# Kernel optimization log

Hardware: AMD Instinct MI355X
Metric: run time of the kernel (lower is better)

The kernel has to match this reference:

```python
import jax, jax.numpy as jnp
import numpy as np
from jax import lax


def _rnn_scan(x, Wih, Whh, bih, bhh):
    """Elman RNN: h_t = tanh(x_t @ Wih^T + bih + h_{t-1} @ Whh^T + bhh).
    x: (B, T, I). Returns (last_hidden (B,H), all_hidden (B,T,H))."""
    B = x.shape[0]
    H = Whh.shape[0]
    xs = jnp.swapaxes(x, 0, 1)  # (T, B, I)
    h0 = jnp.zeros((B, H), dtype=x.dtype)

    def step(h, xt):
        h_new = jnp.tanh(xt @ Wih.T + bih + h @ Whh.T + bhh)
        return h_new, h_new

    last, hs = lax.scan(step, h0, xs)
    return last, jnp.swapaxes(hs, 0, 1)  # (B,H), (B,T,H)


def setup_inputs() -> dict:
    key = jax.random.key(0)
    ks = jax.random.split(key, 12)
    B, T = 4096, 256
    I1, H1, H2 = 1, 5, 100
    s1 = 1.0 / np.sqrt(H1)
    s2 = 1.0 / np.sqrt(H2)
    inp = {
        "x": jax.random.normal(ks[0], (B, T, I1), dtype=jnp.float32),
        "Wih1": jax.random.uniform(ks[1], (H1, I1), jnp.float32, -s1, s1),
        "Whh1": jax.random.uniform(ks[2], (H1, H1), jnp.float32, -s1, s1),
        "bih1": jax.random.uniform(ks[3], (H1,), jnp.float32, -s1, s1),
        "bhh1": jax.random.uniform(ks[4], (H1,), jnp.float32, -s1, s1),
        "Wih2": jax.random.uniform(ks[5], (H2, H1), jnp.float32, -s2, s2),
        "Whh2": jax.random.uniform(ks[6], (H2, H2), jnp.float32, -s2, s2),
        "bih2": jax.random.uniform(ks[7], (H2,), jnp.float32, -s2, s2),
        "bhh2": jax.random.uniform(ks[8], (H2,), jnp.float32, -s2, s2),
        "W3": jax.random.uniform(ks[9], (1, H2), jnp.float32, -s2, s2),
        "b3": jax.random.uniform(ks[10], (1,), jnp.float32, -s2, s2),
    }
    return inp


def reference(x, Wih1, Whh1, bih1, bhh1, Wih2, Whh2, bih2, bhh2, W3, b3):
    # layer_1: out = last hidden (B,5), hidden = full sequence (B,T,5)
    _, h1_seq = _rnn_scan(x, Wih1, Whh1, bih1, bhh1)
    # layer_2 consumes the hidden sequence of layer_1
    out2, _ = _rnn_scan(h1_seq, Wih2, Whh2, bih2, bhh2)  # (B,100)
    # final linear + relu
    return jax.nn.relu(out2 @ W3.T + b3)  # (B,1)
```

## Files before the change

kernel.cpp:

```cpp
#include <hip/hip_runtime.h>
#include <stdint.h>

#define T_STEPS 256
#define H1 5
#define H2 100
#define NSTR 16
#define MT 7
#define KT 4
#define ME 112
#define KE 128
#define XPAD 260
#define NW 8
#define NTHR (NW * 64)

typedef _Float16 f16;
typedef _Float16 half8 __attribute__((ext_vector_type(8)));
typedef _Float16 f16x2 __attribute__((ext_vector_type(2)));
typedef float    floatx4 __attribute__((ext_vector_type(4)));

__device__ __forceinline__ int sidx(int k, int n) {
    return ((k >> 5) << 9) + (((k >> 3) & 3) << 7) + (n << 3) + (k & 7);
}

__device__ __forceinline__ float fast_tanh(float v) {
    float e = __expf(2.0f * v);
    return 1.0f - 2.0f * __builtin_amdgcn_rcpf(e + 1.0f);
}

__device__ __forceinline__ uint32_t pkf16(float a, float b) {
    f16x2 v; v.x = (f16)a; v.y = (f16)b;
    return __builtin_bit_cast(uint32_t, v);
}

__global__ __launch_bounds__(NTHR, 1) void rnn_mfma8(
    const float* __restrict__ x,
    const float* __restrict__ Wih1, const float* __restrict__ Whh1,
    const float* __restrict__ bih1, const float* __restrict__ bhh1,
    const float* __restrict__ Wih2, const float* __restrict__ Whh2,
    const float* __restrict__ bih2, const float* __restrict__ bhh2,
    const float* __restrict__ W3,   const float* __restrict__ b3,
    float* __restrict__ out)
{
    const int tid  = threadIdx.x;
    const int lane = tid & 63;
    const int wid  = tid >> 6;
    const int n    = lane & 15;
    const int g    = lane >> 4;
    const int bbase = blockIdx.x * NSTR;

    __shared__ __align__(16) f16   Wlds[ME][KE];
    __shared__ __align__(16) float xs[NSTR][XPAD];
    __shared__ __align__(16) f16   st[2][2048];
    __shared__ float pp[NW][NSTR];

    {
        uint32_t* w32 = (uint32_t*)&Wlds[0][0];
        #pragma unroll
        for (int i = 0; i < 14; ++i) w32[tid + NTHR * i] = 0u;
        const float4* xg = (const float4*)(x + (size_t)bbase * T_STEPS);
        #pragma unroll
        for (int i = 0; i < 2; ++i) {
            const int gi = tid + NTHR * i;
            *(float4*)&xs[gi >> 6][4 * (gi & 63)] = xg[gi];
        }
    }
    __syncthreads();
    for (int i = tid; i < H2 * H2; i += NTHR) Wlds[i / H2][i % H2] = (f16)Whh2[i];
    for (int i = tid; i < H2 * H1; i += NTHR) Wlds[i / H1][H2 + i % H1] = (f16)Wih2[i];
    for (int i = tid; i < H2; i += NTHR)      Wlds[i][105] = (f16)(bih2[i] + bhh2[i]);
    if (tid < H1 * H1) Wlds[H2 + tid / H1][H2 + tid % H1] = (f16)Whh1[tid];
    if (tid < H1) {
        Wlds[H2 + tid][105] = (f16)(bih1[tid] + bhh1[tid]);
        Wlds[H2 + tid][106] = (f16)Wih1[tid];
    }
    {
        uint32_t* s32 = (uint32_t*)&st[0][0];
        #pragma unroll
        for (int i = 0; i < 4; ++i) s32[tid + NTHR * i] = 0u;
    }
    __syncthreads();
    if (tid < NSTR) {
        const float x0 = xs[tid][0];
        #pragma unroll
        for (int c = 0; c < H1; ++c)
            st[0][sidx(H2 + c, tid)] = (f16)fast_tanh(Wih1[c] * x0 + bih1[c] + bhh1[c]);
        st[0][sidx(105, tid)] = (f16)1.0f;
        st[1][sidx(105, tid)] = (f16)1.0f;
        st[0][sidx(106, tid)] = (f16)xs[tid][1];
    }
    half8 Af[KT];
    if (wid < MT) {
        #pragma unroll
        for (int kt = 0; kt < KT; ++kt)
            Af[kt] = *(const half8*)&Wlds[16 * wid + n][32 * kt + 8 * g];
    }
    __syncthreads();

    const int roff = 16 * lane;
    const int woff = ((wid >> 1) << 10) + (((2 * wid + (g >> 1)) & 3) << 8)
                   + (n << 4) + ((g & 1) << 3);
    char* const sp0 = (char*)&st[0][0];
    char* const sp1 = (char*)&st[1][0];
    uint32_t P0 = 0u, P1 = 0u;

    if (wid == 7) {
        f16* const w0 = &st[0][0];
        f16* const w1 = &st[1][0];
        const int si = sidx(106, n);
        #pragma unroll 1
        for (int t2 = 0; t2 < T_STEPS - 2; t2 += 2) {
            if (lane < NSTR) w1[si] = (f16)xs[n][t2 + 2];
            __syncthreads();
            if (lane < NSTR) w0[si] = (f16)xs[n][t2 + 3 < T_STEPS ? t2 + 3 : T_STEPS - 1];
            __syncthreads();
        }
        if (lane < NSTR) w1[si] = (f16)xs[n][T_STEPS - 1];
        __syncthreads();
    } else {
        auto fullstep = [&](const char* rp, char* wp) {
            half8 Bf[KT];
            #pragma unroll
            for (int kt = 0; kt < KT; ++kt)
                Bf[kt] = *(const half8*)(rp + roff + 1024 * kt);

            __builtin_amdgcn_s_setprio(1);
            floatx4 Da = {0.f, 0.f, 0.f, 0.f}, Db = {0.f, 0.f, 0.f, 0.f};
            Da = __builtin_amdgcn_mfma_f32_16x16x32_f16(Af[0], Bf[0], Da, 0, 0, 0);
            Db = __builtin_amdgcn_mfma_f32_16x16x32_f16(Af[2], Bf[2], Db, 0, 0, 0);
            Da = __builtin_amdgcn_mfma_f32_16x16x32_f16(Af[1], Bf[1], Da, 0, 0, 0);
            Db = __builtin_amdgcn_mfma_f32_16x16x32_f16(Af[3], Bf[3], Db, 0, 0, 0);
            const floatx4 D = Da + Db;

            if (wid < 6 || g < 2) {
                const uint32_t q0 = pkf16(fast_tanh(D[0]), fast_tanh(D[1]));
                const uint32_t q1 = pkf16(fast_tanh(D[2]), fast_tanh(D[3]));
                __builtin_amdgcn_s_setprio(0);
                uint2 w; w.x = q0; w.y = q1;
                *(uint2*)(wp + woff) = w;
            } else if (g == 2) {
                const f16 h4 = (f16)fast_tanh(D[0]);
                __builtin_amdgcn_s_setprio(0);
                *(f16*)(wp + 2 * (1664 + 8 * n)) = h4;
            } else {
                __builtin_amdgcn_s_setprio(0);
            }
            __syncthreads();
        };

        #pragma unroll 1
        for (int t2 = 0; t2 < T_STEPS - 2; t2 += 2) {
            fullstep(sp0, sp1);
            fullstep(sp1, sp0);
        }
        fullstep(sp0, sp1);

        half8 Bf[KT];
        #pragma unroll
        for (int kt = 0; kt < KT; ++kt)
            Bf[kt] = *(const half8*)(sp1 + roff + 1024 * kt);
        floatx4 Da = {0.f, 0.f, 0.f, 0.f}, Db = {0.f, 0.f, 0.f, 0.f};
        Da = __builtin_amdgcn_mfma_f32_16x16x32_f16(Af[0], Bf[0], Da, 0, 0, 0);
        Db = __builtin_amdgcn_mfma_f32_16x16x32_f16(Af[2], Bf[2], Db, 0, 0, 0);
        Da = __builtin_amdgcn_mfma_f32_16x16x32_f16(Af[1], Bf[1], Da, 0, 0, 0);
        Db = __builtin_amdgcn_mfma_f32_16x16x32_f16(Af[3], Bf[3], Db, 0, 0, 0);
        const floatx4 D = Da + Db;
        P0 = pkf16(fast_tanh(D[0]), fast_tanh(D[1]));
        P1 = pkf16(fast_tanh(D[2]), fast_tanh(D[3]));
    }

    float p = 0.0f;
    if (wid < MT) {
        const int mbase = 16 * wid + 4 * g;
        if (mbase < H2) {
            const float4 w3v = *(const float4*)(W3 + mbase);
            const f16x2 lo = __builtin_bit_cast(f16x2, P0);
            const f16x2 hi = __builtin_bit_cast(f16x2, P1);
            p += w3v.x * (float)lo.x + w3v.y * (float)lo.y
               + w3v.z * (float)hi.x + w3v.w * (float)hi.y;
        }
    }
    p += __shfl_xor(p, 16);
    p += __shfl_xor(p, 32);
    if (lane < NSTR) pp[wid][n] = p;
    __syncthreads();
    if (tid < NSTR) {
        float s = b3[0];
        #pragma unroll
        for (int w = 0; w < MT; ++w) s += pp[w][tid];
        out[bbase + tid] = fmaxf(s, 0.0f);
    }
}

extern "C" void kernel_launch(void* const* d_in, const int* in_sizes, int n_in,
                              void* d_out, int out_size, void* d_ws, size_t ws_size,
                              hipStream_t stream) {
    const float* x    = (const float*)d_in[0];
    const float* Wih1 = (const float*)d_in[1];
    const float* Whh1 = (const float*)d_in[2];
    const float* bih1 = (const float*)d_in[3];
    const float* bhh1 = (const float*)d_in[4];
    const float* Wih2 = (const float*)d_in[5];
    const float* Whh2 = (const float*)d_in[6];
    const float* bih2 = (const float*)d_in[7];
    const float* bhh2 = (const float*)d_in[8];
    const float* W3   = (const float*)d_in[9];
    const float* b3   = (const float*)d_in[10];
    float* out = (float*)d_out;

    const int B = in_sizes[0] / T_STEPS;
    rnn_mfma8<<<B / NSTR, NTHR, 0, stream>>>(x, Wih1, Whh1, bih1, bhh1,
                                             Wih2, Whh2, bih2, bhh2, W3, b3, out);
}
```

Measured before the change: 83.90 us.

## Halve waves per block, each wave computing two MFMA row tiles per step

Shrinks the block from 8 waves to 4. Three waves each compute two 16-row output tiles per recurrent step, and the fourth wave computes the last tile (the tail of layer 2 plus layer 1) and also writes the next x value, so the dedicated x-feeder wave is gone. The goal is cheaper per-step __syncthreads across fewer waves and more MFMA work per wave between barriers. In exchange, each wave's critical path per step grows (8 MFMAs plus 8 tanh on the busy waves), and the s_setprio hints are dropped.

```diff
diff --git a/kernel.cpp b/kernel.cpp
--- a/kernel.cpp
+++ b/kernel.cpp
@@ -10,7 +10,7 @@
 #define ME 112
 #define KE 128
 #define XPAD 260
-#define NW 8
+#define NW 4
 #define NTHR (NW * 64)
 
 typedef _Float16 f16;
@@ -32,7 +32,9 @@
     return __builtin_bit_cast(uint32_t, v);
 }
 
-__global__ __launch_bounds__(NTHR, 1) void rnn_mfma8(
+#define MFMA(Aa, Bb, Dd) __builtin_amdgcn_mfma_f32_16x16x32_f16((Aa), (Bb), (Dd), 0, 0, 0)
+
+__global__ __launch_bounds__(NTHR, 1) void rnn_mfma4w(
     const float* __restrict__ x,
     const float* __restrict__ Wih1, const float* __restrict__ Whh1,
     const float* __restrict__ bih1, const float* __restrict__ bhh1,
@@ -56,10 +58,10 @@
     {
         uint32_t* w32 = (uint32_t*)&Wlds[0][0];
         #pragma unroll
-        for (int i = 0; i < 14; ++i) w32[tid + NTHR * i] = 0u;
+        for (int i = 0; i < 28; ++i) w32[tid + NTHR * i] = 0u;
         const float4* xg = (const float4*)(x + (size_t)bbase * T_STEPS);
         #pragma unroll
-        for (int i = 0; i < 2; ++i) {
+        for (int i = 0; i < 4; ++i) {
             const int gi = tid + NTHR * i;
             *(float4*)&xs[gi >> 6][4 * (gi & 63)] = xg[gi];
         }
@@ -76,7 +78,7 @@
     {
         uint32_t* s32 = (uint32_t*)&st[0][0];
         #pragma unroll
-        for (int i = 0; i < 4; ++i) s32[tid + NTHR * i] = 0u;
+        for (int i = 0; i < 8; ++i) s32[tid + NTHR * i] = 0u;
     }
     __syncthreads();
     if (tid < NSTR) {
@@ -88,93 +90,133 @@
         st[1][sidx(105, tid)] = (f16)1.0f;
         st[0][sidx(106, tid)] = (f16)xs[tid][1];
     }
-    half8 Af[KT];
-    if (wid < MT) {
+    const int mt0 = 2 * wid;
+    half8 Af0[KT], Af1[KT];
+    #pragma unroll
+    for (int kt = 0; kt < KT; ++kt)
+        Af0[kt] = *(const half8*)&Wlds[16 * mt0 + n][32 * kt + 8 * g];
+    if (wid < 3) {
         #pragma unroll
         for (int kt = 0; kt < KT; ++kt)
-            Af[kt] = *(const half8*)&Wlds[16 * wid + n][32 * kt + 8 * g];
+            Af1[kt] = *(const half8*)&Wlds[16 * (mt0 + 1) + n][32 * kt + 8 * g];
     }
     __syncthreads();
 
     const int roff = 16 * lane;
-    const int woff = ((wid >> 1) << 10) + (((2 * wid + (g >> 1)) & 3) << 8)
-                   + (n << 4) + ((g & 1) << 3);
+    auto woffof = [&](int mt) {
+        return (((4 * mt + g) >> 3) << 10) + (((2 * mt + (g >> 1)) & 3) << 8)
+             + (n << 4) + ((g & 1) << 3);
+    };
+    const int woff0 = woffof(mt0);
+    const int woff1 = woffof(mt0 + 1);
     char* const sp0 = (char*)&st[0][0];
     char* const sp1 = (char*)&st[1][0];
-    uint32_t P0 = 0u, P1 = 0u;
-
-    if (wid == 7) {
-        f16* const w0 = &st[0][0];
-        f16* const w1 = &st[1][0];
-        const int si = sidx(106, n);
-        #pragma unroll 1
-        for (int t2 = 0; t2 < T_STEPS - 2; t2 += 2) {
-            if (lane < NSTR) w1[si] = (f16)xs[n][t2 + 2];
-            __syncthreads();
-            if (lane < NSTR) w0[si] = (f16)xs[n][t2 + 3 < T_STEPS ? t2 + 3 : T_STEPS - 1];
-            __syncthreads();
-        }
-        if (lane < NSTR) w1[si] = (f16)xs[n][T_STEPS - 1];
-        __syncthreads();
-    } else {
-        auto fullstep = [&](const char* rp, char* wp) {
+    uint32_t P0a = 0u, P1a = 0u, P0b = 0u, P1b = 0u;
+
+    if (wid < 3) {
+        auto step2 = [&](const char* rp, char* wp) {
             half8 Bf[KT];
             #pragma unroll
             for (int kt = 0; kt < KT; ++kt)
                 Bf[kt] = *(const half8*)(rp + roff + 1024 * kt);
-
-            __builtin_amdgcn_s_setprio(1);
-            floatx4 Da = {0.f, 0.f, 0.f, 0.f}, Db = {0.f, 0.f, 0.f, 0.f};
-            Da = __builtin_amdgcn_mfma_f32_16x16x32_f16(Af[0], Bf[0], Da, 0, 0, 0);
-            Db = __builtin_amdgcn_mfma_f32_16x16x32_f16(Af[2], Bf[2], Db, 0, 0, 0);
-            Da = __builtin_amdgcn_mfma_f32_16x16x32_f16(Af[1], Bf[1], Da, 0, 0, 0);
-            Db = __builtin_amdgcn_mfma_f32_16x16x32_f16(Af[3], Bf[3], Db, 0, 0, 0);
+            floatx4 Da = {0.f,0.f,0.f,0.f}, Db = {0.f,0.f,0.f,0.f};
+            floatx4 Dc = {0.f,0.f,0.f,0.f}, Dd = {0.f,0.f,0.f,0.f};
+            Da = MFMA(Af0[0], Bf[0], Da);  Dc = MFMA(Af1[0], Bf[0], Dc);
+            Db = MFMA(Af0[2], Bf[2], Db);  Dd = MFMA(Af1[2], Bf[2], Dd);
+            Da = MFMA(Af0[1], Bf[1], Da);  Dc = MFMA(Af1[1], Bf[1], Dc);
+            Db = MFMA(Af0[3], Bf[3], Db);  Dd = MFMA(Af1[3], Bf[3], Dd);
+            const floatx4 D0 = Da + Db, D1 = Dc + Dd;
+            uint2 w0, w1;
+            w0.x = pkf16(fast_tanh(D0[0]), fast_tanh(D0[1]));
+            w0.y = pkf16(fast_tanh(D0[2]), fast_tanh(D0[3]));
+            w1.x = pkf16(fast_tanh(D1[0]), fast_tanh(D1[1]));
+            w1.y = pkf16(fast_tanh(D1[2]), fast_tanh(D1[3]));
+            *(uint2*)(wp + woff0) = w0;
+            *(uint2*)(wp + woff1) = w1;
+            __syncthreads();
+        };
+        #pragma unroll 1
+        for (int t2 = 0; t2 < T_STEPS - 2; t2 += 2) {
+            step2(sp0, sp1);
+            step2(sp1, sp0);
+        }
+        step2(sp0, sp1);
+        half8 Bf[KT];
+        #pragma unroll
+        for (int kt = 0; kt < KT; ++kt)
+            Bf[kt] = *(const half8*)(sp1 + roff + 1024 * kt);
+        floatx4 Da = {0.f,0.f,0.f,0.f}, Db = {0.f,0.f,0.f,0.f};
+        floatx4 Dc = {0.f,0.f,0.f,0.f}, Dd = {0.f,0.f,0.f,0.f};
+        Da = MFMA(Af0[0], Bf[0], Da);  Dc = MFMA(Af1[0], Bf[0], Dc);
+        Db = MFMA(Af0[2], Bf[2], Db);  Dd = MFMA(Af1[2], Bf[2], Dd);
+        Da = MFMA(Af0[1], Bf[1], Da);  Dc = MFMA(Af1[1], Bf[1], Dc);
+        Db = MFMA(Af0[3], Bf[3], Db);  Dd = MFMA(Af1[3], Bf[3], Dd);
+        const floatx4 D0 = Da + Db, D1 = Dc + Dd;
+        P0a = pkf16(fast_tanh(D0[0]), fast_tanh(D0[1]));
+        P1a = pkf16(fast_tanh(D0[2]), fast_tanh(D0[3]));
+        P0b = pkf16(fast_tanh(D1[0]), fast_tanh(D1[1]));
+        P1b = pkf16(fast_tanh(D1[2]), fast_tanh(D1[3]));
+    } else {
+        auto step1 = [&](const char* rp, char* wp, int t) {
+            const int xi = (t + 2 < T_STEPS) ? (t + 2) : (T_STEPS - 1);
+            const float xv = xs[n][xi];
+            half8 Bf[KT];
+            #pragma unroll
+            for (int kt = 0; kt < KT; ++kt)
+                Bf[kt] = *(const half8*)(rp + roff + 1024 * kt);
+            floatx4 Da = {0.f,0.f,0.f,0.f}, Db = {0.f,0.f,0.f,0.f};
+            Da = MFMA(Af0[0], Bf[0], Da);
+            Db = MFMA(Af0[2], Bf[2], Db);
+            Da = MFMA(Af0[1], Bf[1], Da);
+            Db = MFMA(Af0[3], Bf[3], Db);
             const floatx4 D = Da + Db;
-
-            if (wid < 6 || g < 2) {
-                const uint32_t q0 = pkf16(fast_tanh(D[0]), fast_tanh(D[1]));
-                const uint32_t q1 = pkf16(fast_tanh(D[2]), fast_tanh(D[3]));
-                __builtin_amdgcn_s_setprio(0);
-                uint2 w; w.x = q0; w.y = q1;
-                *(uint2*)(wp + woff) = w;
+            if (g < 2) {
+                uint2 w;
+                w.x = pkf16(fast_tanh(D[0]), fast_tanh(D[1]));
+                w.y = pkf16(fast_tanh(D[2]), fast_tanh(D[3]));
+                *(uint2*)(wp + woff0) = w;
             } else if (g == 2) {
-                const f16 h4 = (f16)fast_tanh(D[0]);
-                __builtin_amdgcn_s_setprio(0);
-                *(f16*)(wp + 2 * (1664 + 8 * n)) = h4;
+                *(f16*)(wp + 2 * (1664 + 8 * n)) = (f16)fast_tanh(D[0]);
             } else {
-                __builtin_amdgcn_s_setprio(0);
+                *(f16*)(wp + 2 * (1666 + 8 * n)) = (f16)xv;
             }
             __syncthreads();
         };
-
         #pragma unroll 1
         for (int t2 = 0; t2 < T_STEPS - 2; t2 += 2) {
-            fullstep(sp0, sp1);
-            fullstep(sp1, sp0);
-        }
-        fullstep(sp0, sp1);
-
+            step1(sp0, sp1, t2);
+            step1(sp1, sp0, t2 + 1);
+        }
+        step1(sp0, sp1, T_STEPS - 2);
         half8 Bf[KT];
         #pragma unroll
         for (int kt = 0; kt < KT; ++kt)
             Bf[kt] = *(const half8*)(sp1 + roff + 1024 * kt);
-        floatx4 Da = {0.f, 0.f, 0.f, 0.f}, Db = {0.f, 0.f, 0.f, 0.f};
-        Da = __builtin_amdgcn_mfma_f32_16x16x32_f16(Af[0], Bf[0], Da, 0, 0, 0);
-        Db = __builtin_amdgcn_mfma_f32_16x16x32_f16(Af[2], Bf[2], Db, 0, 0, 0);
-        Da = __builtin_amdgcn_mfma_f32_16x16x32_f16(Af[1], Bf[1], Da, 0, 0, 0);
-        Db = __builtin_amdgcn_mfma_f32_16x16x32_f16(Af[3], Bf[3], Db, 0, 0, 0);
+        floatx4 Da = {0.f,0.f,0.f,0.f}, Db = {0.f,0.f,0.f,0.f};
+        Da = MFMA(Af0[0], Bf[0], Da);
+        Db = MFMA(Af0[2], Bf[2], Db);
+        Da = MFMA(Af0[1], Bf[1], Da);
+        Db = MFMA(Af0[3], Bf[3], Db);
         const floatx4 D = Da + Db;
-        P0 = pkf16(fast_tanh(D[0]), fast_tanh(D[1]));
-        P1 = pkf16(fast_tanh(D[2]), fast_tanh(D[3]));
+        P0a = pkf16(fast_tanh(D[0]), fast_tanh(D[1]));
+        P1a = pkf16(fast_tanh(D[2]), fast_tanh(D[3]));
     }
 
     float p = 0.0f;
-    if (wid < MT) {
-        const int mbase = 16 * wid + 4 * g;
-        if (mbase < H2) {
-            const float4 w3v = *(const float4*)(W3 + mbase);
-            const f16x2 lo = __builtin_bit_cast(f16x2, P0);
-            const f16x2 hi = __builtin_bit_cast(f16x2, P1);
+    {
+        const int mb0 = 16 * mt0 + 4 * g;
+        if (mb0 < H2) {
+            const float4 w3v = *(const float4*)(W3 + mb0);
+            const f16x2 lo = __builtin_bit_cast(f16x2, P0a);
+            const f16x2 hi = __builtin_bit_cast(f16x2, P1a);
+            p += w3v.x * (float)lo.x + w3v.y * (float)lo.y
+               + w3v.z * (float)hi.x + w3v.w * (float)hi.y;
+        }
+        if (wid < 3) {
+            const int mb1 = 16 * (mt0 + 1) + 4 * g;
+            const float4 w3v = *(const float4*)(W3 + mb1);
+            const f16x2 lo = __builtin_bit_cast(f16x2, P0b);
+            const f16x2 hi = __builtin_bit_cast(f16x2, P1b);
             p += w3v.x * (float)lo.x + w3v.y * (float)lo.y
                + w3v.z * (float)hi.x + w3v.w * (float)hi.y;
         }
@@ -186,7 +228,7 @@
     if (tid < NSTR) {
         float s = b3[0];
         #pragma unroll
-        for (int w = 0; w < MT; ++w) s += pp[w][tid];
+        for (int w = 0; w < NW; ++w) s += pp[w][tid];
         out[bbase + tid] = fmaxf(s, 0.0f);
     }
 }
@@ -208,6 +250,6 @@
     float* out = (float*)d_out;
 
     const int B = in_sizes[0] / T_STEPS;
-    rnn_mfma8<<<B / NSTR, NTHR, 0, stream>>>(x, Wih1, Whh1, bih1, bhh1,
-                                             Wih2, Whh2, bih2, bhh2, W3, b3, out);
-}
+    rnn_mfma4w<<<B / NSTR, NTHR, 0, stream>>>(x, Wih1, Whh1, bih1, bhh1,
+                                              Wih2, Whh2, bih2, bhh2, W3, b3, out);
+}
```

Result: slower. 87.50 us (+4.3%).
